# Performance work log

Measured on AMD Instinct MI355X. Metric: run time of the kernel, lower is better.

## Reference

```python
import jax, jax.numpy as jnp
import numpy as np

N = 100_000      # nodes
E = 1_600_000    # edges (avg degree 16)
F_IN = 128       # in_feats
H = 128          # n_hidden
H2 = 64          # n_hidden // 2


def setup_inputs() -> dict:
    key = jax.random.key(0)
    k1, k2, k3, k4, k5 = jax.random.split(key, 5)
    features = jax.random.normal(k1, (N, F_IN), dtype=jnp.float32)
    W1 = jax.random.normal(k2, (F_IN, H), dtype=jnp.float32) * 0.05
    W2 = jax.random.normal(k3, (H, H2), dtype=jnp.float32) * 0.05
    src = jax.random.randint(k4, (E,), 0, N, dtype=jnp.int32)
    dst = jax.random.randint(k5, (E,), 0, N, dtype=jnp.int32)
    return {"features": features, "W1": W1, "W2": W2, "src": src, "dst": dst}


def _graph_conv(h, W, src, dst, out_norm, in_norm):
    # DGL GraphConv, norm='both', bias=False:
    #   rst = D_dst^{-1/2} * (A @ (D_src^{-1/2} * h)) @ W
    # (weight applied before/after aggregation is mathematically identical)
    h = h * out_norm[:, None]                                   # scale source feats
    agg = jax.ops.segment_sum(h[src], dst, num_segments=N)      # SpMM: sum over in-edges
    return (agg * in_norm[:, None]) @ W


def reference(features, W1, W2, src, dst):
    ones = jnp.ones(src.shape[0], dtype=jnp.float32)
    # allow_zero_in_degree=True -> DGL clamps degrees to min 1 for norm
    out_deg = jnp.clip(jax.ops.segment_sum(ones, src, num_segments=N), 1.0)
    in_deg = jnp.clip(jax.ops.segment_sum(ones, dst, num_segments=N), 1.0)
    out_norm = out_deg ** -0.5
    in_norm = in_deg ** -0.5
    h = _graph_conv(features, W1, src, dst, out_norm, in_norm)  # [N, H]
    h = jax.nn.relu(h)
    return _graph_conv(h, W2, src, dst, out_norm, in_norm)      # [N, H2]
```

## Files before the change

kernel.cpp:

```cpp
#include <hip/hip_runtime.h>
#include <cstdint>
#include <cstddef>

#define NN 100000
#define NE 1600000
#define FD 128
#define HD2 64

#define BSH 7
#define BSZ 128
#define NB ((NN + BSZ - 1) / BSZ)
#define TILE 4096
#define NTILE ((NE + TILE - 1) / TILE)
#define CAPB 2560

static_assert(NB <= 1024, "single-block bucket scan assumes <=1024 buckets");

typedef short bf16x8_t __attribute__((ext_vector_type(8)));
typedef float f32x4_t __attribute__((ext_vector_type(4)));

static __device__ __forceinline__ uint f2bf(float x) {
  uint u = __float_as_uint(x);
  return (u + 0x7fffu + ((u >> 16) & 1u)) >> 16;
}
static __device__ __forceinline__ uint pack2(float lo, float hi) {
  return f2bf(lo) | (f2bf(hi) << 16);
}
static __device__ __forceinline__ float bflo(uint v) { return __uint_as_float(v << 16); }
static __device__ __forceinline__ float bfhi(uint v) { return __uint_as_float(v & 0xffff0000u); }

__global__ void k_bucket(const int* __restrict__ src, const int* __restrict__ dst,
                         int* __restrict__ bcnt_d, int* __restrict__ bcnt_s,
                         uint* __restrict__ brec_d, ushort* __restrict__ brec_s) {
  __shared__ int hd[NB], gbd[NB], hs[NB], gbs[NB];
  for (int i = threadIdx.x; i < NB; i += 256) { hd[i] = 0; hs[i] = 0; }
  __syncthreads();
  int base = blockIdx.x * TILE;
  for (int i = threadIdx.x; i < TILE; i += 256) {
    int e = base + i;
    if (e < NE) {
      atomicAdd(&hd[dst[e] >> BSH], 1);
      atomicAdd(&hs[src[e] >> BSH], 1);
    }
  }
  __syncthreads();
  for (int i = threadIdx.x; i < NB; i += 256) {
    int cd = hd[i], cs = hs[i];
    gbd[i] = cd ? atomicAdd(bcnt_d + i, cd) : 0;
    gbs[i] = cs ? atomicAdd(bcnt_s + i, cs) : 0;
    hd[i] = 0;
    hs[i] = 0;
  }
  __syncthreads();
  for (int i = threadIdx.x; i < TILE; i += 256) {
    int e = base + i;
    if (e < NE) {
      int d = dst[e], sv = src[e];
      int bd = d >> BSH, bs = sv >> BSH;
      int rd = gbd[bd] + atomicAdd(&hd[bd], 1);
      if (rd < CAPB)
        brec_d[(size_t)bd * CAPB + rd] = ((uint)(d & (BSZ - 1)) << 17) | (uint)sv;
      int rs = gbs[bs] + atomicAdd(&hs[bs], 1);
      if (rs < CAPB)
        brec_s[(size_t)bs * CAPB + rs] = (ushort)(sv & (BSZ - 1));
    }
  }
}

__global__ __launch_bounds__(1024) void k_bscan(const int* __restrict__ bcnt_d,
                                                int* __restrict__ boff_d) {
  __shared__ int s[1024];
  int t = threadIdx.x;
  int v = (t < NB) ? bcnt_d[t] : 0;
  s[t] = v;
  __syncthreads();
#pragma unroll
  for (int off = 1; off < 1024; off <<= 1) {
    int x = (t >= off) ? s[t - off] : 0;
    __syncthreads();
    s[t] += x;
    __syncthreads();
  }
  if (t < NB) boff_d[t + 1] = s[t];
  if (t == 0) boff_d[0] = 0;
}

__global__ __launch_bounds__(256) void k_build_dst(const uint* __restrict__ brec,
                                                   const int* __restrict__ bcnt,
                                                   const int* __restrict__ boff,
                                                   int* __restrict__ row_ptr,
                                                   float* __restrict__ in_norm,
                                                   int* __restrict__ csr) {
  __shared__ int lcnt[BSZ];
  __shared__ int lscan[BSZ + 1];
  __shared__ int lcur[BSZ];
  __shared__ int lcsr[CAPB];
  const int t = threadIdx.x;
  const int b = blockIdx.x;
  const int d0 = b * BSZ;
  const int nd = min(BSZ, NN - d0);
  const int len = min(bcnt[b], CAPB);
  const size_t rbase = (size_t)b * CAPB;
  const int ebase = boff[b];

  for (int i = t; i < BSZ; i += 256) lcnt[i] = 0;
  __syncthreads();
  for (int e = t; e < len; e += 256)
    atomicAdd(&lcnt[brec[rbase + e] >> 17], 1);
  __syncthreads();

  for (int i = t; i < nd; i += 256)
    in_norm[d0 + i] = rsqrtf((float)max(lcnt[i], 1));

  if (t < BSZ) lcur[t] = lcnt[t];
  __syncthreads();
#pragma unroll
  for (int off = 1; off < BSZ; off <<= 1) {
    int x = (t >= off && t < BSZ) ? lcur[t - off] : 0;
    __syncthreads();
    if (t < BSZ) lcur[t] += x;
    __syncthreads();
  }
  if (t < BSZ) lscan[t + 1] = lcur[t];
  if (t == 0) lscan[0] = 0;
  __syncthreads();
  for (int i = t; i <= nd; i += 256) row_ptr[d0 + i] = ebase + lscan[i];
  if (t < BSZ) lcur[t] = lscan[t];
  __syncthreads();

  for (int e = t; e < len; e += 256) {
    uint r = brec[rbase + e];
    int p = atomicAdd(&lcur[r >> 17], 1);
    lcsr[p] = (int)(r & 0x1FFFFu);
  }
  __syncthreads();
  for (int ld = t; ld < nd; ld += 256) {
    int a = lscan[ld], bnd = lscan[ld + 1];
    for (int i = a + 1; i < bnd; ++i) {
      int v = lcsr[i];
      int j = i - 1;
      while (j >= a && lcsr[j] > v) { lcsr[j + 1] = lcsr[j]; --j; }
      lcsr[j + 1] = v;
    }
  }
  __syncthreads();
  for (int i = t; i < len; i += 256) csr[ebase + i] = lcsr[i];
}

__global__ void k_build_src(const ushort* __restrict__ brec,
                            const int* __restrict__ bcnt,
                            float* __restrict__ out_norm) {
  __shared__ int lcnt[BSZ];
  const int t = threadIdx.x;
  const int b = blockIdx.x;
  const int s0 = b * BSZ;
  const int ns = min(BSZ, NN - s0);
  const int len = min(bcnt[b], CAPB);
  const size_t rbase = (size_t)b * CAPB;
  for (int i = t; i < BSZ; i += 256) lcnt[i] = 0;
  __syncthreads();
  for (int e = t; e < len; e += 256)
    atomicAdd(&lcnt[brec[rbase + e]], 1);
  __syncthreads();
  for (int i = t; i < ns; i += 256)
    out_norm[s0 + i] = rsqrtf((float)max(lcnt[i], 1));
}

__global__ void k_prescale(const float* __restrict__ feat, const float* __restrict__ onorm,
                           uint* __restrict__ Xb) {
  int t = blockIdx.x * 256 + threadIdx.x;
  int row = t >> 6, j = t & 63;
  float2 f = *(const float2*)(feat + (size_t)row * FD + 2 * j);
  float w = onorm[row];
  Xb[t] = pack2(f.x * w, f.y * w);
}

__global__ void k_wt(const float* __restrict__ W1, const float* __restrict__ W2,
                     uint* __restrict__ W1t, uint* __restrict__ W2t) {
  int i = blockIdx.x * 256 + threadIdx.x;
  if (i < FD * 64) {
    int n = i >> 6, kk = i & 63;
    W1t[i] = pack2(W1[(size_t)(2 * kk) * FD + n], W1[(size_t)(2 * kk + 1) * FD + n]);
  } else {
    int i2 = i - FD * 64;
    int n = i2 >> 6, kk = i2 & 63;
    W2t[i2] = pack2(W2[(size_t)(2 * kk) * HD2 + n], W2[(size_t)(2 * kk + 1) * HD2 + n]);
  }
}

__global__ void k_spmm1b(const uint* __restrict__ Xb, const int* __restrict__ row_ptr,
                         const int* __restrict__ csr_src, const float* __restrict__ in_norm,
                         uint* __restrict__ Hb1) {
  int gid = blockIdx.x * blockDim.x + threadIdx.x;
  int row = gid >> 6;
  if (row >= NN) return;
  int lane = threadIdx.x & 63;
  int grp = lane >> 4;
  int gl = lane & 15;
  int e0 = row_ptr[row], e1 = row_ptr[row + 1];
  float2 a0 = {0.f, 0.f}, a1 = {0.f, 0.f}, a2 = {0.f, 0.f}, a3 = {0.f, 0.f};
#define ACC1(v)                                  \
  a0.x += bflo((v).x); a0.y += bfhi((v).x);      \
  a1.x += bflo((v).y); a1.y += bfhi((v).y);      \
  a2.x += bflo((v).z); a2.y += bfhi((v).z);      \
  a3.x += bflo((v).w); a3.y += bfhi((v).w);
  int e = e0;
  for (; e + 8 <= e1; e += 8) {
    int s0 = csr_src[e + grp];
    int s1 = csr_src[e + 4 + grp];
    uint4 v0 = *(const uint4*)(Xb + ((size_t)s0 << 6) + (gl << 2));
    uint4 v1 = *(const uint4*)(Xb + ((size_t)s1 << 6) + (gl << 2));
    ACC1(v0);
    ACC1(v1);
  }
  for (; e + 4 <= e1; e += 4) {
    int s0 = csr_src[e + grp];
    uint4 v0 = *(const uint4*)(Xb + ((size_t)s0 << 6) + (gl << 2));
    ACC1(v0);
  }
  if (e + grp < e1) {
    int s0 = csr_src[e + grp];
    uint4 v0 = *(const uint4*)(Xb + ((size_t)s0 << 6) + (gl << 2));
    ACC1(v0);
  }
#undef ACC1
#pragma unroll
  for (int m = 16; m <= 32; m <<= 1) {
    a0.x += __shfl_xor(a0.x, m); a0.y += __shfl_xor(a0.y, m);
    a1.x += __shfl_xor(a1.x, m); a1.y += __shfl_xor(a1.y, m);
    a2.x += __shfl_xor(a2.x, m); a2.y += __shfl_xor(a2.y, m);
    a3.x += __shfl_xor(a3.x, m); a3.y += __shfl_xor(a3.y, m);
  }
  if (grp == 0) {
    float wi = in_norm[row];
    uint4 o;
    o.x = pack2(a0.x * wi, a0.y * wi);
    o.y = pack2(a1.x * wi, a1.y * wi);
    o.z = pack2(a2.x * wi, a2.y * wi);
    o.w = pack2(a3.x * wi, a3.y * wi);
    *(uint4*)(Hb1 + ((size_t)row << 6) + (gl << 2)) = o;
  }
}

__global__ __launch_bounds__(256) void k_mlp(const uint* __restrict__ Hb1,
                                             const uint* __restrict__ W1t,
                                             const uint* __restrict__ W2t,
                                             const float* __restrict__ onorm,
                                             ushort* __restrict__ Tb) {
  __shared__ ushort h_lds[64 * FD];
  char* const lds = (char*)h_lds;
  const int tid = threadIdx.x;
  const int wid = tid >> 6;
  const int lane = tid & 63;
  const int l15 = lane & 15;
  const int g = lane >> 4;
  const int rowbase = blockIdx.x * 64 + wid * 16;

  const int ar = min(rowbase + l15, NN - 1);
  const uint* Arow = Hb1 + (size_t)ar * 64;
  bf16x8_t afr[4];
#pragma unroll
  for (int kc = 0; kc < 4; ++kc)
    afr[kc] = *(const bf16x8_t*)(Arow + kc * 16 + g * 4);

  float wnorm[4];
#pragma unroll
  for (int r = 0; r < 4; ++r)
    wnorm[r] = onorm[min(rowbase + 4 * g + r, NN - 1)];

#pragma unroll
  for (int nf = 0; nf < 8; ++nf) {
    f32x4_t acc = {0.f, 0.f, 0.f, 0.f};
#pragma unroll
    for (int kc = 0; kc < 4; ++kc) {
      bf16x8_t b = *(const bf16x8_t*)(W1t + (size_t)(nf * 16 + l15) * 64 + kc * 16 + g * 4);
      acc = __builtin_amdgcn_mfma_f32_16x16x32_bf16(afr[kc], b, acc, 0, 0, 0);
    }
#pragma unroll
    for (int r = 0; r < 4; ++r) {
      float hv = fmaxf(acc[r], 0.f) * wnorm[r];
      int row = wid * 16 + 4 * g + r;
      int byte = row * 256 + (nf * 16 + l15) * 2;
      byte ^= (row & 7) << 4;
      *(ushort*)(lds + byte) = (ushort)f2bf(hv);
    }
  }
  __syncthreads();

  bf16x8_t a2[4];
#pragma unroll
  for (int kc = 0; kc < 4; ++kc) {
    int row = wid * 16 + l15;
    int byte = row * 256 + (kc * 32 + 8 * g) * 2;
    byte ^= (row & 7) << 4;
    a2[kc] = *(const bf16x8_t*)(lds + byte);
  }
#pragma unroll
  for (int nf = 0; nf < 4; ++nf) {
    f32x4_t acc = {0.f, 0.f, 0.f, 0.f};
#pragma unroll
    for (int kc = 0; kc < 4; ++kc) {
      bf16x8_t b = *(const bf16x8_t*)(W2t + (size_t)(nf * 16 + l15) * 64 + kc * 16 + g * 4);
      acc = __builtin_amdgcn_mfma_f32_16x16x32_bf16(a2[kc], b, acc, 0, 0, 0);
    }
#pragma unroll
    for (int r = 0; r < 4; ++r) {
      int row = rowbase + 4 * g + r;
      if (row < NN)
        Tb[(size_t)row * HD2 + nf * 16 + l15] = (ushort)f2bf(acc[r]);
    }
  }
}

__global__ void k_spmm2b(const uint* __restrict__ Tb, const int* __restrict__ row_ptr,
                         const int* __restrict__ csr_src, const float* __restrict__ in_norm,
                         float* __restrict__ out) {
  int gid = blockIdx.x * blockDim.x + threadIdx.x;
  int row = gid >> 6;
  if (row >= NN) return;
  int lane = threadIdx.x & 63;
  int grp = lane >> 3;
  int gl = lane & 7;
  int e0 = row_ptr[row], e1 = row_ptr[row + 1];
  float2 a0 = {0.f, 0.f}, a1 = {0.f, 0.f}, a2 = {0.f, 0.f}, a3 = {0.f, 0.f};
#define ACC2(v)                                  \
  a0.x += bflo((v).x); a0.y += bfhi((v).x);      \
  a1.x += bflo((v).y); a1.y += bfhi((v).y);      \
  a2.x += bflo((v).z); a2.y += bfhi((v).z);      \
  a3.x += bflo((v).w); a3.y += bfhi((v).w);
  int e = e0;
  for (; e + 16 <= e1; e += 16) {
    int s0 = csr_src[e + grp];
    int s1 = csr_src[e + 8 + grp];
    uint4 v0 = *(const uint4*)(Tb + ((size_t)s0 << 5) + (gl << 2));
    uint4 v1 = *(const uint4*)(Tb + ((size_t)s1 << 5) + (gl << 2));
    ACC2(v0);
    ACC2(v1);
  }
  for (; e + 8 <= e1; e += 8) {
    int s0 = csr_src[e + grp];
    uint4 v0 = *(const uint4*)(Tb + ((size_t)s0 << 5) + (gl << 2));
    ACC2(v0);
  }
  if (e + grp < e1) {
    int s0 = csr_src[e + grp];
    uint4 v0 = *(const uint4*)(Tb + ((size_t)s0 << 5) + (gl << 2));
    ACC2(v0);
  }
#undef ACC2
#pragma unroll
  for (int m = 8; m <= 32; m <<= 1) {
    a0.x += __shfl_xor(a0.x, m); a0.y += __shfl_xor(a0.y, m);
    a1.x += __shfl_xor(a1.x, m); a1.y += __shfl_xor(a1.y, m);
    a2.x += __shfl_xor(a2.x, m); a2.y += __shfl_xor(a2.y, m);
    a3.x += __shfl_xor(a3.x, m); a3.y += __shfl_xor(a3.y, m);
  }
  if (lane < 8) {
    float wi = in_norm[row];
    float* orow = out + (size_t)row * HD2 + gl * 8;
    *(float4*)orow = make_float4(a0.x * wi, a0.y * wi, a1.x * wi, a1.y * wi);
    *(float4*)(orow + 4) = make_float4(a2.x * wi, a2.y * wi, a3.x * wi, a3.y * wi);
  }
}

extern "C" void kernel_launch(void* const* d_in, const int* in_sizes, int n_in,
                              void* d_out, int out_size, void* d_ws, size_t ws_size,
                              hipStream_t stream) {
  const float* feat = (const float*)d_in[0];
  const float* W1   = (const float*)d_in[1];
  const float* W2   = (const float*)d_in[2];
  const int*   src  = (const int*)d_in[3];
  const int*   dst  = (const int*)d_in[4];
  float* out = (float*)d_out;

  char* p = (char*)d_ws;
  auto take = [&p](size_t bytes) -> char* {
    char* r = p;
    p += (bytes + 511) & ~(size_t)511;
    return r;
  };
  int*   row_ptr  = (int*)take((size_t)(NN + 1) * 4);
  int*   bcnt     = (int*)take((size_t)2 * NB * 4);
  int*   boff_d   = (int*)take((size_t)(NB + 1) * 4);
  float* out_norm = (float*)take((size_t)NN * 4);
  float* in_norm  = (float*)take((size_t)NN * 4);
  int*   csr_src  = (int*)take((size_t)NE * 4);
  uint*  W1t      = (uint*)take((size_t)FD * 64 * 4);
  uint*  W2t      = (uint*)take((size_t)HD2 * 64 * 4);
  uint*  Xb       = (uint*)take((size_t)NN * 64 * 4);
  uint*  Hb1      = (uint*)take((size_t)NN * 64 * 4);
  int*   bcnt_d   = bcnt;
  int*   bcnt_s   = bcnt + NB;
  ushort* Tb      = (ushort*)Xb;
  uint*   brec_d  = (uint*)Hb1;
  ushort* brec_s  = (ushort*)(Hb1 + (size_t)NB * CAPB);

  hipMemsetAsync(bcnt, 0, (size_t)2 * NB * 4, stream);

  k_bucket   <<<NTILE, 256, 0, stream>>>(src, dst, bcnt_d, bcnt_s, brec_d, brec_s);
  k_bscan    <<<1, 1024, 0, stream>>>(bcnt_d, boff_d);
  k_build_dst<<<NB, 256, 0, stream>>>(brec_d, bcnt_d, boff_d, row_ptr, in_norm, csr_src);
  k_build_src<<<NB, 256, 0, stream>>>(brec_s, bcnt_s, out_norm);

  k_prescale<<<(NN * 64) / 256, 256, 0, stream>>>(feat, out_norm, Xb);
  k_wt      <<<(FD * 64 + HD2 * 64) / 256, 256, 0, stream>>>(W1, W2, W1t, W2t);

  k_spmm1b<<<(NN * 64) / 256, 256, 0, stream>>>(Xb, row_ptr, csr_src, in_norm, Hb1);
  k_mlp   <<<(NN + 63) / 64, 256, 0, stream>>>(Hb1, W1t, W2t, out_norm, Tb);
  k_spmm2b<<<(NN * 64) / 256, 256, 0, stream>>>((const uint*)Tb, row_ptr, csr_src, in_norm, out);
}
```

Measured before the change: 275.4 us.

## Merge build and prep kernels, deepen SpMM unroll, narrow SpMM2 gather width

Folds the source-degree counting into the destination CSR build kernel, and the feature prescale into the weight-transpose kernel, cutting two launches. Unrolls the first SpMM edge loop to 16 edges per iteration to keep more gathers in flight. Restructures the second SpMM so 16 lanes each load 8 bytes per edge instead of 8 lanes loading 16 bytes, which means 4 edges in flight per step and fewer accumulators. Risks are higher register pressure in the first SpMM and smaller memory transactions in the second.

```diff
diff --git a/kernel.cpp b/kernel.cpp
--- a/kernel.cpp
+++ b/kernel.cpp
@@ -85,12 +85,15 @@
   if (t == 0) boff_d[0] = 0;
 }
 
-__global__ __launch_bounds__(256) void k_build_dst(const uint* __restrict__ brec,
-                                                   const int* __restrict__ bcnt,
-                                                   const int* __restrict__ boff,
-                                                   int* __restrict__ row_ptr,
-                                                   float* __restrict__ in_norm,
-                                                   int* __restrict__ csr) {
+__global__ __launch_bounds__(256) void k_build(const uint* __restrict__ brec_d,
+                                               const ushort* __restrict__ brec_s,
+                                               const int* __restrict__ bcnt_d,
+                                               const int* __restrict__ bcnt_s,
+                                               const int* __restrict__ boff,
+                                               int* __restrict__ row_ptr,
+                                               float* __restrict__ in_norm,
+                                               float* __restrict__ out_norm,
+                                               int* __restrict__ csr) {
   __shared__ int lcnt[BSZ];
   __shared__ int lscan[BSZ + 1];
   __shared__ int lcur[BSZ];
@@ -99,16 +102,15 @@
   const int b = blockIdx.x;
   const int d0 = b * BSZ;
   const int nd = min(BSZ, NN - d0);
-  const int len = min(bcnt[b], CAPB);
   const size_t rbase = (size_t)b * CAPB;
+
+  const int len = min(bcnt_d[b], CAPB);
   const int ebase = boff[b];
-
   for (int i = t; i < BSZ; i += 256) lcnt[i] = 0;
   __syncthreads();
   for (int e = t; e < len; e += 256)
-    atomicAdd(&lcnt[brec[rbase + e] >> 17], 1);
-  __syncthreads();
-
+    atomicAdd(&lcnt[brec_d[rbase + e] >> 17], 1);
+  __syncthreads();
   for (int i = t; i < nd; i += 256)
     in_norm[d0 + i] = rsqrtf((float)max(lcnt[i], 1));
 
@@ -129,7 +131,7 @@
   __syncthreads();
 
   for (int e = t; e < len; e += 256) {
-    uint r = brec[rbase + e];
+    uint r = brec_d[rbase + e];
     int p = atomicAdd(&lcur[r >> 17], 1);
     lcsr[p] = (int)(r & 0x1FFFFu);
   }
@@ -145,46 +147,38 @@
   }
   __syncthreads();
   for (int i = t; i < len; i += 256) csr[ebase + i] = lcsr[i];
-}
-
-__global__ void k_build_src(const ushort* __restrict__ brec,
-                            const int* __restrict__ bcnt,
-                            float* __restrict__ out_norm) {
-  __shared__ int lcnt[BSZ];
-  const int t = threadIdx.x;
-  const int b = blockIdx.x;
-  const int s0 = b * BSZ;
-  const int ns = min(BSZ, NN - s0);
-  const int len = min(bcnt[b], CAPB);
-  const size_t rbase = (size_t)b * CAPB;
+
+  __syncthreads();
   for (int i = t; i < BSZ; i += 256) lcnt[i] = 0;
   __syncthreads();
-  for (int e = t; e < len; e += 256)
-    atomicAdd(&lcnt[brec[rbase + e]], 1);
-  __syncthreads();
-  for (int i = t; i < ns; i += 256)
-    out_norm[s0 + i] = rsqrtf((float)max(lcnt[i], 1));
-}
-
-__global__ void k_prescale(const float* __restrict__ feat, const float* __restrict__ onorm,
-                           uint* __restrict__ Xb) {
+  const int len_s = min(bcnt_s[b], CAPB);
+  for (int e = t; e < len_s; e += 256)
+    atomicAdd(&lcnt[brec_s[rbase + e]], 1);
+  __syncthreads();
+  for (int i = t; i < nd; i += 256)
+    out_norm[d0 + i] = rsqrtf((float)max(lcnt[i], 1));
+}
+
+__global__ void k_prep(const float* __restrict__ feat, const float* __restrict__ onorm,
+                       uint* __restrict__ Xb,
+                       const float* __restrict__ W1, const float* __restrict__ W2,
+                       uint* __restrict__ W1t, uint* __restrict__ W2t) {
   int t = blockIdx.x * 256 + threadIdx.x;
-  int row = t >> 6, j = t & 63;
-  float2 f = *(const float2*)(feat + (size_t)row * FD + 2 * j);
-  float w = onorm[row];
-  Xb[t] = pack2(f.x * w, f.y * w);
-}
-
-__global__ void k_wt(const float* __restrict__ W1, const float* __restrict__ W2,
-                     uint* __restrict__ W1t, uint* __restrict__ W2t) {
-  int i = blockIdx.x * 256 + threadIdx.x;
-  if (i < FD * 64) {
-    int n = i >> 6, kk = i & 63;
-    W1t[i] = pack2(W1[(size_t)(2 * kk) * FD + n], W1[(size_t)(2 * kk + 1) * FD + n]);
+  if (t < NN * 64) {
+    int row = t >> 6, j = t & 63;
+    float2 f = *(const float2*)(feat + (size_t)row * FD + 2 * j);
+    float w = onorm[row];
+    Xb[t] = pack2(f.x * w, f.y * w);
   } else {
-    int i2 = i - FD * 64;
-    int n = i2 >> 6, kk = i2 & 63;
-    W2t[i2] = pack2(W2[(size_t)(2 * kk) * HD2 + n], W2[(size_t)(2 * kk + 1) * HD2 + n]);
+    int i = t - NN * 64;
+    if (i < FD * 64) {
+      int n = i >> 6, kk = i & 63;
+      W1t[i] = pack2(W1[(size_t)(2 * kk) * FD + n], W1[(size_t)(2 * kk + 1) * FD + n]);
+    } else {
+      int i2 = i - FD * 64;
+      int n = i2 >> 6, kk = i2 & 63;
+      W2t[i2] = pack2(W2[(size_t)(2 * kk) * HD2 + n], W2[(size_t)(2 * kk + 1) * HD2 + n]);
+    }
   }
 }
 
@@ -205,13 +199,19 @@
   a2.x += bflo((v).z); a2.y += bfhi((v).z);      \
   a3.x += bflo((v).w); a3.y += bfhi((v).w);
   int e = e0;
-  for (; e + 8 <= e1; e += 8) {
+  for (; e + 16 <= e1; e += 16) {
     int s0 = csr_src[e + grp];
     int s1 = csr_src[e + 4 + grp];
+    int s2 = csr_src[e + 8 + grp];
+    int s3 = csr_src[e + 12 + grp];
     uint4 v0 = *(const uint4*)(Xb + ((size_t)s0 << 6) + (gl << 2));
     uint4 v1 = *(const uint4*)(Xb + ((size_t)s1 << 6) + (gl << 2));
+    uint4 v2 = *(const uint4*)(Xb + ((size_t)s2 << 6) + (gl << 2));
+    uint4 v3 = *(const uint4*)(Xb + ((size_t)s3 << 6) + (gl << 2));
     ACC1(v0);
     ACC1(v1);
+    ACC1(v2);
+    ACC1(v3);
   }
   for (; e + 4 <= e1; e += 4) {
     int s0 = csr_src[e + grp];
@@ -319,47 +319,48 @@
   int row = gid >> 6;
   if (row >= NN) return;
   int lane = threadIdx.x & 63;
-  int grp = lane >> 3;
-  int gl = lane & 7;
+  int grp = lane >> 4;
+  int gl = lane & 15;
   int e0 = row_ptr[row], e1 = row_ptr[row + 1];
-  float2 a0 = {0.f, 0.f}, a1 = {0.f, 0.f}, a2 = {0.f, 0.f}, a3 = {0.f, 0.f};
+  float2 a0 = {0.f, 0.f}, a1 = {0.f, 0.f};
 #define ACC2(v)                                  \
   a0.x += bflo((v).x); a0.y += bfhi((v).x);      \
-  a1.x += bflo((v).y); a1.y += bfhi((v).y);      \
-  a2.x += bflo((v).z); a2.y += bfhi((v).z);      \
-  a3.x += bflo((v).w); a3.y += bfhi((v).w);
+  a1.x += bflo((v).y); a1.y += bfhi((v).y);
   int e = e0;
   for (; e + 16 <= e1; e += 16) {
     int s0 = csr_src[e + grp];
-    int s1 = csr_src[e + 8 + grp];
-    uint4 v0 = *(const uint4*)(Tb + ((size_t)s0 << 5) + (gl << 2));
-    uint4 v1 = *(const uint4*)(Tb + ((size_t)s1 << 5) + (gl << 2));
+    int s1 = csr_src[e + 4 + grp];
+    int s2 = csr_src[e + 8 + grp];
+    int s3 = csr_src[e + 12 + grp];
+    uint2 v0 = *(const uint2*)(Tb + ((size_t)s0 << 5) + (gl << 1));
+    uint2 v1 = *(const uint2*)(Tb + ((size_t)s1 << 5) + (gl << 1));
+    uint2 v2 = *(const uint2*)(Tb + ((size_t)s2 << 5) + (gl << 1));
+    uint2 v3 = *(const uint2*)(Tb + ((size_t)s3 << 5) + (gl << 1));
     ACC2(v0);
     ACC2(v1);
-  }
-  for (; e + 8 <= e1; e += 8) {
-    int s0 = csr_src[e + grp];
-    uint4 v0 = *(const uint4*)(Tb + ((size_t)s0 << 5) + (gl << 2));
+    ACC2(v2);
+    ACC2(v3);
+  }
+  for (; e + 4 <= e1; e += 4) {
+    int s0 = csr_src[e + grp];
+    uint2 v0 = *(const uint2*)(Tb + ((size_t)s0 << 5) + (gl << 1));
     ACC2(v0);
   }
   if (e + grp < e1) {
     int s0 = csr_src[e + grp];
-    uint4 v0 = *(const uint4*)(Tb + ((size_t)s0 << 5) + (gl << 2));
+    uint2 v0 = *(const uint2*)(Tb + ((size_t)s0 << 5) + (gl << 1));
     ACC2(v0);
   }
 #undef ACC2
 #pragma unroll
-  for (int m = 8; m <= 32; m <<= 1) {
+  for (int m = 16; m <= 32; m <<= 1) {
     a0.x += __shfl_xor(a0.x, m); a0.y += __shfl_xor(a0.y, m);
     a1.x += __shfl_xor(a1.x, m); a1.y += __shfl_xor(a1.y, m);
-    a2.x += __shfl_xor(a2.x, m); a2.y += __shfl_xor(a2.y, m);
-    a3.x += __shfl_xor(a3.x, m); a3.y += __shfl_xor(a3.y, m);
-  }
-  if (lane < 8) {
+  }
+  if (grp == 0) {
     float wi = in_norm[row];
-    float* orow = out + (size_t)row * HD2 + gl * 8;
-    *(float4*)orow = make_float4(a0.x * wi, a0.y * wi, a1.x * wi, a1.y * wi);
-    *(float4*)(orow + 4) = make_float4(a2.x * wi, a2.y * wi, a3.x * wi, a3.y * wi);
+    *(float4*)(out + (size_t)row * HD2 + gl * 4) =
+        make_float4(a0.x * wi, a0.y * wi, a1.x * wi, a1.y * wi);
   }
 }
 
@@ -397,13 +398,12 @@
 
   hipMemsetAsync(bcnt, 0, (size_t)2 * NB * 4, stream);
 
-  k_bucket   <<<NTILE, 256, 0, stream>>>(src, dst, bcnt_d, bcnt_s, brec_d, brec_s);
-  k_bscan    <<<1, 1024, 0, stream>>>(bcnt_d, boff_d);
-  k_build_dst<<<NB, 256, 0, stream>>>(brec_d, bcnt_d, boff_d, row_ptr, in_norm, csr_src);
-  k_build_src<<<NB, 256, 0, stream>>>(brec_s, bcnt_s, out_norm);
-
-  k_prescale<<<(NN * 64) / 256, 256, 0, stream>>>(feat, out_norm, Xb);
-  k_wt      <<<(FD * 64 + HD2 * 64) / 256, 256, 0, stream>>>(W1, W2, W1t, W2t);
+  k_bucket<<<NTILE, 256, 0, stream>>>(src, dst, bcnt_d, bcnt_s, brec_d, brec_s);
+  k_bscan <<<1, 1024, 0, stream>>>(bcnt_d, boff_d);
+  k_build <<<NB, 256, 0, stream>>>(brec_d, brec_s, bcnt_d, bcnt_s, boff_d,
+                                   row_ptr, in_norm, out_norm, csr_src);
+  k_prep  <<<(NN * 64 + FD * 64 + HD2 * 64) / 256, 256, 0, stream>>>(feat, out_norm, Xb,
+                                                                     W1, W2, W1t, W2t);
 
   k_spmm1b<<<(NN * 64) / 256, 256, 0, stream>>>(Xb, row_ptr, csr_src, in_norm, Hb1);
   k_mlp   <<<(NN + 63) / 64, 256, 0, stream>>>(Hb1, W1t, W2t, out_norm, Tb);
```

New measurement: 276.2 us. Within noise of the previous version (+0.3%).
